# Performance work log

Measured on AMD Instinct MI355X. Metric: run time of the kernel, lower is better.

The kernel has to match this reference:

```python
import jax, jax.numpy as jnp
import numpy as np

BATCH, IN_DIM, GRID, HID, DEPTH = 2048, 128, 128, 256, 7
BN_EPS = 1e-5


def setup_inputs() -> dict:
    key = jax.random.key(0)
    ks = jax.random.split(key, 10)
    x = jax.random.uniform(ks[0], (BATCH, IN_DIM), dtype=jnp.float32)
    grids = jax.random.uniform(ks[1], (DEPTH, IN_DIM, GRID), dtype=jnp.float32)  # torch.rand init
    fs = jax.random.normal(ks[2], (DEPTH, IN_DIM, GRID, HID), dtype=jnp.float32)
    depth_scores = jnp.ones((DEPTH,), dtype=jnp.float32)
    mlp_W = jax.random.normal(ks[3], (3, HID, HID), dtype=jnp.float32) * (1.0 / np.sqrt(HID))
    mlp_b = jnp.zeros((3, HID), dtype=jnp.float32)
    bn_gamma = jnp.ones((3, HID), dtype=jnp.float32)
    bn_beta = jnp.zeros((3, HID), dtype=jnp.float32)
    W_out = jax.random.normal(ks[4], (HID, 1), dtype=jnp.float32) * (1.0 / np.sqrt(HID))
    b_out = jnp.zeros((1,), dtype=jnp.float32)
    return {"x": x, "grids": grids, "fs": fs, "depth_scores": depth_scores,
            "mlp_W": mlp_W, "mlp_b": mlp_b, "bn_gamma": bn_gamma,
            "bn_beta": bn_beta, "W_out": W_out, "b_out": b_out}


def reference(x, grids, fs, depth_scores, mlp_W, mlp_b, bn_gamma, bn_beta, W_out, b_out):
    # per-feature min-max normalization over the batch dim
    xmin = x.min(axis=0, keepdims=True)
    xmax = x.max(axis=0, keepdims=True)
    z = (x - xmin) / (xmax - xmin + 1e-6)  # [B, I]

    outputs = []
    for i in range(DEPTH):
        Bmat = jax.nn.relu(z[:, :, None] - grids[i][None, :, :])  # [B, I, G]
        # (B.unsqueeze(-1) * fs[i]).sum(2).sum(1) == einsum big,igh->bh
        H = jnp.einsum('big,igh->bh', Bmat, fs[i])  # [B, H]
        if i > 0:  # residual accumulation
            H = H + outputs[-1]
        outputs.append(H)
    stacked = jnp.stack(outputs, axis=0)  # [D, B, H]
    w = jax.nn.softmax(depth_scores)  # depth attention
    h = jnp.einsum('d,dbh->bh', w, stacked)

    # MLP head (BatchNorm uses batch stats = training-mode behaviour; Dropout off)
    for j in range(3):
        h = h @ mlp_W[j] + mlp_b[j]
        mean = h.mean(axis=0)
        var = h.var(axis=0)  # biased, matching torch BN normalization
        h = (h - mean) * jax.lax.rsqrt(var + BN_EPS) * bn_gamma[j] + bn_beta[j]
        h = jax.nn.gelu(h, approximate=False)  # torch nn.GELU is exact erf GELU
    return h @ W_out + b_out
```

## Files before the change

kernel.cpp:

```cpp
#include <hip/hip_runtime.h>
#include <hip/hip_bf16.h>

#define BATCH 2048
#define IN_DIM 128
#define GRIDN 128
#define HID 256
#define DEPTH 7

typedef unsigned int u32;
typedef __attribute__((ext_vector_type(8))) short short8;
typedef __attribute__((ext_vector_type(4))) float floatx4;

#define OFF_FST   ((size_t)0)
#define SZ_FST    ((size_t)7*128*256*128*2)
#define OFF_ZT    (OFF_FST + SZ_FST)
#define SZ_ZT     ((size_t)BATCH*IN_DIM*4)
#define OFF_HPRE  (OFF_ZT + SZ_ZT)
#define SZ_HPRE   ((size_t)BATCH*HID*4)
#define OFF_STATS (OFF_HPRE + SZ_HPRE)
#define SZ_STATS  ((size_t)3*2*HID*4)
#define OFF_KEYS  (OFF_STATS + SZ_STATS)
#define SZ_KEYS   ((size_t)256*4)
#define OFF_CW    (OFF_KEYS + SZ_KEYS)
#define SZ_CW     ((size_t)32)
#define OFF_Y1    (OFF_CW + SZ_CW)
#define SZ_Y      ((size_t)BATCH*HID*4)
#define OFF_Y2    (OFF_Y1 + SZ_Y)
#define OFF_Y3    (OFF_Y2 + SZ_Y)

#define FENCE __asm__ volatile("" ::: "memory")
#define WAITV(c) do { __builtin_amdgcn_s_waitcnt(c); FENCE; } while (0)
#define BARR do { FENCE; __builtin_amdgcn_s_barrier(); FENCE; } while (0)
#define VM8 0x0F78
#define VM0 0x0F70

__device__ __forceinline__ void gload_lds16(const void* g, void* l) {
  __builtin_amdgcn_global_load_lds(
      (const __attribute__((address_space(1))) u32*)g,
      (__attribute__((address_space(3))) u32*)l, 16, 0, 0);
}

__device__ __forceinline__ u32 pack2_bf16(float lo, float hi) {
  __hip_bfloat162 b2;
  b2.x = __float2bfloat16(lo);
  b2.y = __float2bfloat16(hi);
  return *reinterpret_cast<u32*>(&b2);
}

__device__ __forceinline__ u32 pk_trunc(float a, float b) {
  return __builtin_amdgcn_perm(__float_as_uint(b), __float_as_uint(a), 0x07060302u);
}

__device__ __forceinline__ float reluc(float v) {
  return __builtin_amdgcn_fmed3f(v, 0.0f, 1.0f);
}

__device__ __forceinline__ float gelu_exact(float x) {
  return 0.5f * x * (1.0f + erff(x * 0.70710678118654752f));
}

__global__ void prep1_kernel(const float* __restrict__ x, u32* __restrict__ keys,
                             const float* __restrict__ depth_scores,
                             float* __restrict__ cw) {
  int t = threadIdx.x;
  int base = blockIdx.x * 256 + t;
  float mn = 1e30f, mx = -1e30f;
#pragma unroll
  for (int j = 0; j < 16; ++j) {
    float v = x[base + j * 16384];
    mn = fminf(mn, v); mx = fmaxf(mx, v);
  }
  __shared__ float smn[256], smx[256];
  smn[t] = mn; smx[t] = mx;
  __syncthreads();
  if (t < 128) {
    mn = fminf(smn[t], smn[t + 128]);
    mx = fmaxf(smx[t], smx[t + 128]);
    int i = base & 127;
    atomicMax(&keys[i], 0x7FFFFFFFu - __float_as_uint(mn));
    atomicMax(&keys[128 + i], __float_as_uint(mx));
  }
  if (blockIdx.x == 0 && t == 0) {
    float m = -1e30f;
    for (int d0 = 0; d0 < DEPTH; ++d0) m = fmaxf(m, depth_scores[d0]);
    float e[DEPTH]; float sum = 0.f;
    for (int d0 = 0; d0 < DEPTH; ++d0) { e[d0] = expf(depth_scores[d0] - m); sum += e[d0]; }
    float cacc = 0.f; float cs[DEPTH];
    for (int d0 = DEPTH - 1; d0 >= 0; --d0) { cacc += e[d0] / sum; cs[d0] = cacc; }
    for (int d0 = 0; d0 < DEPTH; ++d0) cw[d0] = cs[d0];
  }
}

__global__ void prep2_kernel(const float* __restrict__ x, const u32* __restrict__ keys,
                             float* __restrict__ z_t) {
  __shared__ float lds[128 * 65];
  int t = threadIdx.x;
  int b0 = blockIdx.x * 64;
#pragma unroll
  for (int q = 0; q < 32; ++q) {
    int idx = q * 256 + t;
    int b = idx >> 7, i = idx & 127;
    lds[i * 65 + b] = x[(size_t)(b0 + b) * IN_DIM + i];
  }
  __syncthreads();
#pragma unroll
  for (int q = 0; q < 32; ++q) {
    int idx = q * 256 + t;
    int ii = idx >> 6, bb = idx & 63;
    float mnv = __uint_as_float(0x7FFFFFFFu - keys[ii]);
    float mxv = __uint_as_float(keys[128 + ii]);
    float v = (lds[ii * 65 + bb] - mnv) * (1.0f / (mxv - mnv + 1e-6f));
    z_t[(size_t)ii * BATCH + b0 + bb] = v;
  }
}

__global__ void convert_kernel(const float* __restrict__ fs,
                               const float* __restrict__ cw,
                               __hip_bfloat16* __restrict__ fs2) {
  __shared__ __align__(16) float lds[32 * 256];
  int slab = blockIdx.x;
  int t = threadIdx.x;
  int w = t >> 6, l = t & 63;
  float cd = cw[slab >> 7];
  const float* src = fs + (size_t)slab * (GRIDN * HID);
  char* dstb = (char*)fs2 + (size_t)slab * 65536;

  for (int ks = 0; ks < 4; ++ks) {
    const float* s0 = src + (size_t)ks * 32 * HID;
#pragma unroll
    for (int i = 0; i < 8; ++i) {
      int r = w * 8 + i;
      int mask = ((r >> 3) & 3) << 3;
      gload_lds16(s0 + (size_t)r * HID + ((l * 4) ^ mask),
                  (char*)lds + r * 1024);
    }
    WAITV(VM0);
    BARR;
#pragma unroll
    for (int it = 0; it < 4; ++it) {
      int task = t + it * 256;
      int nhalf = task >> 9;
      int q = task & 511;
      int tt = q >> 6, l4 = (q >> 4) & 3, l15 = q & 15;
      int h = nhalf * 128 + tt * 16 + l15;
      int msk = l4 << 3;
      int hx = h ^ msk;
      uint4 pk4;
      {
        float a0 = lds[(l4 * 8 + 0) * 256 + hx];
        float b0 = lds[(l4 * 8 + 1) * 256 + hx];
        float a1 = lds[(l4 * 8 + 2) * 256 + hx];
        float b1 = lds[(l4 * 8 + 3) * 256 + hx];
        float a2 = lds[(l4 * 8 + 4) * 256 + hx];
        float b2 = lds[(l4 * 8 + 5) * 256 + hx];
        float a3 = lds[(l4 * 8 + 6) * 256 + hx];
        float b3 = lds[(l4 * 8 + 7) * 256 + hx];
        pk4.x = pack2_bf16(cd * a0, cd * b0);
        pk4.y = pack2_bf16(cd * a1, cd * b1);
        pk4.z = pack2_bf16(cd * a2, cd * b2);
        pk4.w = pack2_bf16(cd * a3, cd * b3);
      }
      size_t off = (size_t)nhalf * 32768 + (size_t)ks * 8192 +
                   (size_t)tt * 1024 + l4 * 256 + l15 * 16;
      *(uint4*)(dstb + off) = pk4;
    }
    BARR;
  }
}

__launch_bounds__(256, 2)
__global__ void gemm_kernel(const float* __restrict__ z_t,
                            const float* __restrict__ grids,
                            const __hip_bfloat16* __restrict__ fs2,
                            float* __restrict__ h_pre) {
  __shared__ __align__(16) char lds[24576];

  int bx = blockIdx.x;
  int xcd = bx & 7;
  int t6 = bx >> 3;
  int cg2 = t6 >> 4;
  int jb2 = t6 & 15;
  int chunk = xcd + 8 * cg2;
  int slab0 = chunk * 28;
  int mt = jb2 >> 1;
  int nh = jb2 & 1;

  int tid = threadIdx.x;
  int w = tid >> 6, l = tid & 63;
  int l15 = l & 15, l4 = l >> 4;
  int mbase = mt * 256 + w * 64;
  int nbase = nh * 128;

  floatx4 acc[4][8];
#pragma unroll
  for (int a = 0; a < 4; ++a)
#pragma unroll
    for (int b = 0; b < 8; ++b) acc[a][b] = (floatx4)0.f;

  const char* fsb = (const char*)fs2 + (size_t)slab0 * 65536 + (size_t)nh * 32768 +
                    (size_t)w * 2048 + (size_t)l * 16;

  auto stage8 = [&](int u, int bufIdx) {
    const char* srcb = fsb + (size_t)(u >> 2) * 65536 + (size_t)(u & 3) * 8192;
    char* dst = lds + bufIdx * 8192 + w * 2048;
    gload_lds16(srcb, dst);
    gload_lds16(srcb + 1024, dst + 1024);
  };

  float4 zA, zB;
  float4 g0A, g1A, g0B, g1B;
  auto zgload = [&](int s, float4& zv, float4& G0, float4& G1) {
    int slab = slab0 + (s >> 2);
    int iz = slab & 127;
    const float* zp = z_t + (size_t)iz * BATCH + mbase + l15;
    zv.x = zp[0]; zv.y = zp[16]; zv.z = zp[32]; zv.w = zp[48];
    const float* gp = grids + (size_t)slab * GRIDN + (s & 3) * 32 + l4 * 8;
    G0 = *(const float4*)gp;
    G1 = *(const float4*)(gp + 4);
  };

  short8 af[4];
  short8 bf[8];
  auto rdfrag8 = [&](int bufIdx) {
    const char* bp = lds + bufIdx * 8192 + l * 16;
#pragma unroll
    for (int tt = 0; tt < 8; ++tt)
      bf[tt] = *(const short8*)(bp + tt * 1024);
  };
  auto afgen = [&](const float4 zv, const float4 G0, const float4 G1) {
#pragma unroll
    for (int u = 0; u < 4; ++u) {
      float zu = (u == 0) ? zv.x : (u == 1) ? zv.y : (u == 2) ? zv.z : zv.w;
      union { uint4 q; short8 s8; } pk;
      pk.q.x = pk_trunc(reluc(zu - G0.x), reluc(zu - G0.y));
      pk.q.y = pk_trunc(reluc(zu - G0.z), reluc(zu - G0.w));
      pk.q.z = pk_trunc(reluc(zu - G1.x), reluc(zu - G1.y));
      pk.q.w = pk_trunc(reluc(zu - G1.z), reluc(zu - G1.w));
      af[u] = pk.s8;
    }
  };
  auto mfma32 = [&]() {
    __builtin_amdgcn_s_setprio(1);
#pragma unroll
    for (int u = 0; u < 4; ++u)
#pragma unroll
      for (int tt = 0; tt < 8; ++tt)
        acc[u][tt] = __builtin_amdgcn_mfma_f32_16x16x32_bf16(af[u], bf[tt], acc[u][tt], 0, 0, 0);
    __builtin_amdgcn_s_setprio(0);
  };

#define STEP_FULL(S, BUF, STBUF, ZV, G0, G1)                                   \
  do {                                                                         \
    WAITV(VM8); BARR;                                                          \
    stage8((S) + 2, (STBUF)); FENCE;                                           \
    rdfrag8(BUF);                                                              \
    afgen(ZV, G0, G1);                                                         \
    zgload((S) + 2, ZV, G0, G1); FENCE;                                        \
    mfma32();                                                                  \
  } while (0)

  stage8(0, 0); FENCE;
  zgload(0, zA, g0A, g1A); FENCE;
  stage8(1, 1); FENCE;
  zgload(1, zB, g0B, g1B); FENCE;

#pragma unroll 1
  for (int s0 = 0; s0 < 108; s0 += 6) {
    STEP_FULL(s0 + 0, 0, 2, zA, g0A, g1A);
    STEP_FULL(s0 + 1, 1, 0, zB, g0B, g1B);
    STEP_FULL(s0 + 2, 2, 1, zA, g0A, g1A);
    STEP_FULL(s0 + 3, 0, 2, zB, g0B, g1B);
    STEP_FULL(s0 + 4, 1, 0, zA, g0A, g1A);
    STEP_FULL(s0 + 5, 2, 1, zB, g0B, g1B);
  }

  STEP_FULL(108, 0, 2, zA, g0A, g1A);
  STEP_FULL(109, 1, 0, zB, g0B, g1B);
  WAITV(VM8); BARR;
  rdfrag8(2);
  afgen(zA, g0A, g1A);
  mfma32();
  WAITV(VM0); BARR;
  rdfrag8(0);
  afgen(zB, g0B, g1B);
  mfma32();

  int row0 = mbase + l4 * 4;
  int col0 = nbase + l15;
#pragma unroll
  for (int u = 0; u < 4; ++u) {
#pragma unroll
    for (int tt = 0; tt < 8; ++tt) {
      int col = col0 + tt * 16;
#pragma unroll
      for (int r = 0; r < 4; ++r) {
        int row = row0 + u * 16 + r;
        atomicAdd(&h_pre[(size_t)row * HID + col], acc[u][tt][r]);
      }
    }
  }
}

template <int FIRST>
__global__ void mlp_kernel(const float* __restrict__ Xin,
                           const float* __restrict__ statsIn,
                           const float* __restrict__ gamma,
                           const float* __restrict__ beta,
                           const float* __restrict__ W,
                           const float* __restrict__ bias,
                           float* __restrict__ Yout,
                           float* __restrict__ statsOut) {
  __shared__ float Xs[4][HID];
  int br = blockIdx.x, c = threadIdx.x;
  float mean = 0.f, rstd = 1.f, gm = 1.f, bt = 0.f;
  if (!FIRST) {
    float s1 = statsIn[c], s2 = statsIn[HID + c];
    mean = s1 * (1.0f / BATCH);
    float var = s2 * (1.0f / BATCH) - mean * mean;
    rstd = rsqrtf(var + 1e-5f);
    gm = gamma[c]; bt = beta[c];
  }
#pragma unroll
  for (int r = 0; r < 4; ++r) {
    float v = Xin[(size_t)(br * 4 + r) * HID + c];
    if (!FIRST) v = gelu_exact((v - mean) * rstd * gm + bt);
    Xs[r][c] = v;
  }
  __syncthreads();
  float acc[4] = {0, 0, 0, 0};
#pragma unroll 8
  for (int k = 0; k < HID; ++k) {
    float wv = W[(size_t)k * HID + c];
#pragma unroll
    for (int r = 0; r < 4; ++r) acc[r] += Xs[r][k] * wv;
  }
  float bb = bias[c];
  float s1 = 0.f, s2 = 0.f;
#pragma unroll
  for (int r = 0; r < 4; ++r) {
    float y = acc[r] + bb;
    Yout[(size_t)(br * 4 + r) * HID + c] = y;
    s1 += y; s2 += y * y;
  }
  atomicAdd(&statsOut[c], s1);
  atomicAdd(&statsOut[HID + c], s2);
}

__global__ void final_kernel(const float* __restrict__ Y3,
                             const float* __restrict__ statsIn,
                             const float* __restrict__ gamma,
                             const float* __restrict__ beta,
                             const float* __restrict__ W_out,
                             const float* __restrict__ b_out,
                             float* __restrict__ out) {
  int w = threadIdx.x >> 6, l = threadIdx.x & 63;
  int b = blockIdx.x * 4 + w;
  float4 y = *(const float4*)(Y3 + (size_t)b * HID + l * 4);
  float4 wv = *(const float4*)(W_out + l * 4);
  float r4[4] = {y.x, y.y, y.z, y.w};
  float w4[4] = {wv.x, wv.y, wv.z, wv.w};
  float s = 0.f;
  int c0 = l * 4;
#pragma unroll
  for (int q = 0; q < 4; ++q) {
    int c = c0 + q;
    float s1 = statsIn[c], s2 = statsIn[HID + c];
    float mean = s1 * (1.0f / BATCH);
    float var = s2 * (1.0f / BATCH) - mean * mean;
    float rstd = rsqrtf(var + 1e-5f);
    float v = gelu_exact((r4[q] - mean) * rstd * gamma[c] + beta[c]);
    s += v * w4[q];
  }
#pragma unroll
  for (int off = 32; off > 0; off >>= 1) s += __shfl_down(s, off);
  if (l == 0) out[b] = s + b_out[0];
}

extern "C" void kernel_launch(void* const* d_in, const int* in_sizes, int n_in,
                              void* d_out, int out_size, void* d_ws, size_t ws_size,
                              hipStream_t stream) {
  const float* x      = (const float*)d_in[0];
  const float* grids  = (const float*)d_in[1];
  const float* fs     = (const float*)d_in[2];
  const float* dscore = (const float*)d_in[3];
  const float* mlp_W  = (const float*)d_in[4];
  const float* mlp_b  = (const float*)d_in[5];
  const float* bn_g   = (const float*)d_in[6];
  const float* bn_b   = (const float*)d_in[7];
  const float* W_out  = (const float*)d_in[8];
  const float* b_out  = (const float*)d_in[9];
  float* out = (float*)d_out;

  char* ws = (char*)d_ws;
  __hip_bfloat16* fs2 = (__hip_bfloat16*)(ws + OFF_FST);
  float* z_t   = (float*)(ws + OFF_ZT);
  float* h_pre = (float*)(ws + OFF_HPRE);
  float* stats = (float*)(ws + OFF_STATS);
  u32*   keys  = (u32*)(ws + OFF_KEYS);
  float* cw    = (float*)(ws + OFF_CW);
  float* Y1    = (float*)(ws + OFF_Y1);
  float* Y2    = (float*)(ws + OFF_Y2);
  float* Y3    = (float*)(ws + OFF_Y3);

  hipMemsetAsync(h_pre, 0, SZ_HPRE + SZ_STATS + SZ_KEYS, stream);

  prep1_kernel<<<64, 256, 0, stream>>>(x, keys, dscore, cw);
  prep2_kernel<<<32, 256, 0, stream>>>(x, keys, z_t);
  convert_kernel<<<DEPTH * IN_DIM, 256, 0, stream>>>(fs, cw, fs2);
  gemm_kernel<<<512, 256, 0, stream>>>(z_t, grids, fs2, h_pre);

  mlp_kernel<1><<<512, 256, 0, stream>>>(h_pre, nullptr, nullptr, nullptr,
                                         mlp_W, mlp_b, Y1, stats);
  mlp_kernel<0><<<512, 256, 0, stream>>>(Y1, stats, bn_g, bn_b,
                                         mlp_W + 65536, mlp_b + 256, Y2, stats + 512);
  mlp_kernel<0><<<512, 256, 0, stream>>>(Y2, stats + 512, bn_g + 256, bn_b + 256,
                                         mlp_W + 2 * 65536, mlp_b + 2 * 256, Y3, stats + 1024);
  final_kernel<<<512, 256, 0, stream>>>(Y3, stats + 1024, bn_g + 512, bn_b + 512,
                                        W_out, b_out, out);
}
```

Measured before the change: 425.2 us.

## Halve GEMM block tile to 128x128 and double grid for more occupancy

Each GEMM block now covers 128 rows by 128 columns instead of 256 by 128. The four waves are arranged as a 2x2 grid of 64x64 subtiles, and the launch grows from 512 to 1024 blocks. Accumulators drop from 32 to 16 floatx4, and launch bounds ask for 3 blocks per CU, aiming at more parallelism and better latency hiding. The cost is that each staged B tile is reused by half as many rows, so the bf16 fs weight stream is read twice as often overall, with more global and L2 traffic per MFMA.

```diff
diff --git a/kernel.cpp b/kernel.cpp
--- a/kernel.cpp
+++ b/kernel.cpp
@@ -168,7 +168,7 @@
   }
 }
 
-__launch_bounds__(256, 2)
+__launch_bounds__(256, 3)
 __global__ void gemm_kernel(const float* __restrict__ z_t,
                             const float* __restrict__ grids,
                             const __hip_bfloat16* __restrict__ fs2,
@@ -178,8 +178,8 @@
   int bx = blockIdx.x;
   int xcd = bx & 7;
   int t6 = bx >> 3;
-  int cg2 = t6 >> 4;
-  int jb2 = t6 & 15;
+  int cg2 = t6 >> 5;
+  int jb2 = t6 & 31;
   int chunk = xcd + 8 * cg2;
   int slab0 = chunk * 28;
   int mt = jb2 >> 1;
@@ -188,14 +188,16 @@
   int tid = threadIdx.x;
   int w = tid >> 6, l = tid & 63;
   int l15 = l & 15, l4 = l >> 4;
-  int mbase = mt * 256 + w * 64;
-  int nbase = nh * 128;
-
-  floatx4 acc[4][8];
+  int wm = w >> 1;
+  int wn2 = w & 1;
+  int mbase = mt * 128 + wm * 64;
+  int nbase = nh * 128 + wn2 * 64;
+
+  floatx4 acc[4][4];
 #pragma unroll
   for (int a = 0; a < 4; ++a)
 #pragma unroll
-    for (int b = 0; b < 8; ++b) acc[a][b] = (floatx4)0.f;
+    for (int b = 0; b < 4; ++b) acc[a][b] = (floatx4)0.f;
 
   const char* fsb = (const char*)fs2 + (size_t)slab0 * 65536 + (size_t)nh * 32768 +
                     (size_t)w * 2048 + (size_t)l * 16;
@@ -220,12 +222,12 @@
   };
 
   short8 af[4];
-  short8 bf[8];
-  auto rdfrag8 = [&](int bufIdx) {
-    const char* bp = lds + bufIdx * 8192 + l * 16;
-#pragma unroll
-    for (int tt = 0; tt < 8; ++tt)
-      bf[tt] = *(const short8*)(bp + tt * 1024);
+  short8 bf[4];
+  auto rdfrag4 = [&](int bufIdx) {
+    const char* bp = lds + bufIdx * 8192 + wn2 * 4096 + l * 16;
+#pragma unroll
+    for (int j = 0; j < 4; ++j)
+      bf[j] = *(const short8*)(bp + j * 1024);
   };
   auto afgen = [&](const float4 zv, const float4 G0, const float4 G1) {
 #pragma unroll
@@ -239,13 +241,13 @@
       af[u] = pk.s8;
     }
   };
-  auto mfma32 = [&]() {
+  auto mfma16 = [&]() {
     __builtin_amdgcn_s_setprio(1);
 #pragma unroll
     for (int u = 0; u < 4; ++u)
 #pragma unroll
-      for (int tt = 0; tt < 8; ++tt)
-        acc[u][tt] = __builtin_amdgcn_mfma_f32_16x16x32_bf16(af[u], bf[tt], acc[u][tt], 0, 0, 0);
+      for (int j = 0; j < 4; ++j)
+        acc[u][j] = __builtin_amdgcn_mfma_f32_16x16x32_bf16(af[u], bf[j], acc[u][j], 0, 0, 0);
     __builtin_amdgcn_s_setprio(0);
   };
 
@@ -253,10 +255,10 @@
   do {                                                                         \
     WAITV(VM8); BARR;                                                          \
     stage8((S) + 2, (STBUF)); FENCE;                                           \
-    rdfrag8(BUF);                                                              \
+    rdfrag4(BUF);                                                              \
     afgen(ZV, G0, G1);                                                         \
     zgload((S) + 2, ZV, G0, G1); FENCE;                                        \
-    mfma32();                                                                  \
+    mfma16();                                                                  \
   } while (0)
 
   stage8(0, 0); FENCE;
@@ -277,25 +279,25 @@
   STEP_FULL(108, 0, 2, zA, g0A, g1A);
   STEP_FULL(109, 1, 0, zB, g0B, g1B);
   WAITV(VM8); BARR;
-  rdfrag8(2);
+  rdfrag4(2);
   afgen(zA, g0A, g1A);
-  mfma32();
+  mfma16();
   WAITV(VM0); BARR;
-  rdfrag8(0);
+  rdfrag4(0);
   afgen(zB, g0B, g1B);
-  mfma32();
+  mfma16();
 
   int row0 = mbase + l4 * 4;
   int col0 = nbase + l15;
 #pragma unroll
   for (int u = 0; u < 4; ++u) {
 #pragma unroll
-    for (int tt = 0; tt < 8; ++tt) {
-      int col = col0 + tt * 16;
+    for (int j = 0; j < 4; ++j) {
+      int col = col0 + j * 16;
 #pragma unroll
       for (int r = 0; r < 4; ++r) {
         int row = row0 + u * 16 + r;
-        atomicAdd(&h_pre[(size_t)row * HID + col], acc[u][tt][r]);
+        atomicAdd(&h_pre[(size_t)row * HID + col], acc[u][j][r]);
       }
     }
   }
@@ -407,7 +409,7 @@
   prep1_kernel<<<64, 256, 0, stream>>>(x, keys, dscore, cw);
   prep2_kernel<<<32, 256, 0, stream>>>(x, keys, z_t);
   convert_kernel<<<DEPTH * IN_DIM, 256, 0, stream>>>(fs, cw, fs2);
-  gemm_kernel<<<512, 256, 0, stream>>>(z_t, grids, fs2, h_pre);
+  gemm_kernel<<<1024, 256, 0, stream>>>(z_t, grids, fs2, h_pre);
 
   mlp_kernel<1><<<512, 256, 0, stream>>>(h_pre, nullptr, nullptr, nullptr,
                                          mlp_W, mlp_b, Y1, stats);
```

Measured after the change: 433.1 us. Within noise of the previous version (+1.8%).

## Fuse min-max prep into convert kernel and triple-buffer fs conversion loads

Applied to the files above, without the earlier changes.

Merges the min/max reduction kernel into the fs-to-bf16 conversion kernel as extra blocks, and has each conversion block compute its own softmax tail weight instead of reading it from a prior kernel. The conversion loop is restructured from four synchronous 32-row phases into eight 16-row phases with a three-slot LDS ring, so global-to-LDS loads overlap with the bf16 packing work. This removes one launch and a serial dependency, and aims to hide memory latency in a bandwidth-bound conversion of the large fs tensor. The cost is redundant per-block softmax math and more barriers per block.

```diff
diff --git a/kernel.cpp b/kernel.cpp
--- a/kernel.cpp
+++ b/kernel.cpp
@@ -32,6 +32,7 @@
 #define WAITV(c) do { __builtin_amdgcn_s_waitcnt(c); FENCE; } while (0)
 #define BARR do { FENCE; __builtin_amdgcn_s_barrier(); FENCE; } while (0)
 #define VM8 0x0F78
+#define VM4 0x0F74
 #define VM0 0x0F70
 
 __device__ __forceinline__ void gload_lds16(const void* g, void* l) {
@@ -59,36 +60,99 @@
   return 0.5f * x * (1.0f + erff(x * 0.70710678118654752f));
 }
 
-__global__ void prep1_kernel(const float* __restrict__ x, u32* __restrict__ keys,
-                             const float* __restrict__ depth_scores,
-                             float* __restrict__ cw) {
+__global__ void convert_prep1_kernel(const float* __restrict__ fs,
+                                     const float* __restrict__ depth_scores,
+                                     const float* __restrict__ x,
+                                     u32* __restrict__ keys,
+                                     __hip_bfloat16* __restrict__ fs2) {
+  __shared__ __align__(16) float lds3[3 * 16 * 256];
+  int bid = blockIdx.x;
   int t = threadIdx.x;
-  int base = blockIdx.x * 256 + t;
-  float mn = 1e30f, mx = -1e30f;
-#pragma unroll
-  for (int j = 0; j < 16; ++j) {
-    float v = x[base + j * 16384];
-    mn = fminf(mn, v); mx = fmaxf(mx, v);
-  }
-  __shared__ float smn[256], smx[256];
-  smn[t] = mn; smx[t] = mx;
-  __syncthreads();
-  if (t < 128) {
-    mn = fminf(smn[t], smn[t + 128]);
-    mx = fmaxf(smx[t], smx[t + 128]);
-    int i = base & 127;
-    atomicMax(&keys[i], 0x7FFFFFFFu - __float_as_uint(mn));
-    atomicMax(&keys[128 + i], __float_as_uint(mx));
-  }
-  if (blockIdx.x == 0 && t == 0) {
-    float m = -1e30f;
-    for (int d0 = 0; d0 < DEPTH; ++d0) m = fmaxf(m, depth_scores[d0]);
-    float e[DEPTH]; float sum = 0.f;
-    for (int d0 = 0; d0 < DEPTH; ++d0) { e[d0] = expf(depth_scores[d0] - m); sum += e[d0]; }
-    float cacc = 0.f; float cs[DEPTH];
-    for (int d0 = DEPTH - 1; d0 >= 0; --d0) { cacc += e[d0] / sum; cs[d0] = cacc; }
-    for (int d0 = 0; d0 < DEPTH; ++d0) cw[d0] = cs[d0];
-  }
+
+  if (bid >= DEPTH * IN_DIM) {
+    int pb = bid - DEPTH * IN_DIM;
+    int base = pb * 256 + t;
+    float mn = 1e30f, mx = -1e30f;
+#pragma unroll
+    for (int j = 0; j < 16; ++j) {
+      float v = x[base + j * 16384];
+      mn = fminf(mn, v); mx = fmaxf(mx, v);
+    }
+    float* smn = lds3; float* smx = lds3 + 256;
+    smn[t] = mn; smx[t] = mx;
+    __syncthreads();
+    if (t < 128) {
+      mn = fminf(smn[t], smn[t + 128]);
+      mx = fmaxf(smx[t], smx[t + 128]);
+      int i = base & 127;
+      atomicMax(&keys[i], 0x7FFFFFFFu - __float_as_uint(mn));
+      atomicMax(&keys[128 + i], __float_as_uint(mx));
+    }
+    return;
+  }
+
+  int slab = bid;
+  int w = t >> 6, l = t & 63;
+  int d = slab >> 7;
+  float m = -1e30f; float ds[DEPTH];
+#pragma unroll
+  for (int i = 0; i < DEPTH; ++i) { ds[i] = depth_scores[i]; m = fmaxf(m, ds[i]); }
+  float sum = 0.f, tail = 0.f;
+#pragma unroll
+  for (int i = 0; i < DEPTH; ++i) {
+    float e = expf(ds[i] - m);
+    sum += e;
+    if (i >= d) tail += e;
+  }
+  float cd = tail / sum;
+
+  const float* src = fs + (size_t)slab * (GRIDN * HID);
+  char* dstb = (char*)fs2 + (size_t)slab * 65536;
+
+  auto dmaPhase = [&](int p) {
+    const float* s0 = src + (size_t)p * 16 * HID;
+    char* bb = (char*)lds3 + (p % 3) * 16384;
+#pragma unroll
+    for (int i = 0; i < 4; ++i) {
+      int sl = w * 4 + i;
+      int r = p * 16 + sl;
+      int mask = ((r >> 3) & 3) << 3;
+      gload_lds16(s0 + (size_t)sl * HID + ((l * 4) ^ mask), bb + sl * 1024);
+    }
+  };
+  auto packPhase = [&](int p) {
+    int ks = p >> 1, hh = p & 1;
+    const float* bb = lds3 + (p % 3) * 4096;
+#pragma unroll
+    for (int it = 0; it < 2; ++it) {
+      int task = t + it * 256;
+      int nhalf = task >> 8;
+      int q = task & 255;
+      int tt = q >> 5, l4h = (q >> 4) & 1, l15 = q & 15;
+      int l4 = hh * 2 + l4h;
+      int hgl = nhalf * 128 + tt * 16 + l15;
+      int hx = hgl ^ (l4 << 3);
+      const float* rp = bb + (l4h * 8) * 256 + hx;
+      uint4 pk4;
+      pk4.x = pack2_bf16(cd * rp[0 * 256], cd * rp[1 * 256]);
+      pk4.y = pack2_bf16(cd * rp[2 * 256], cd * rp[3 * 256]);
+      pk4.z = pack2_bf16(cd * rp[4 * 256], cd * rp[5 * 256]);
+      pk4.w = pack2_bf16(cd * rp[6 * 256], cd * rp[7 * 256]);
+      size_t off = (size_t)nhalf * 32768 + (size_t)ks * 8192 +
+                   (size_t)tt * 1024 + (size_t)l4 * 256 + (size_t)l15 * 16;
+      *(uint4*)(dstb + off) = pk4;
+    }
+  };
+
+  dmaPhase(0); dmaPhase(1); FENCE;
+#pragma unroll 1
+  for (int p = 0; p < 6; ++p) {
+    WAITV(VM4); BARR;
+    dmaPhase(p + 2); FENCE;
+    packPhase(p);
+  }
+  WAITV(VM4); BARR; packPhase(6);
+  WAITV(VM0); BARR; packPhase(7);
 }
 
 __global__ void prep2_kernel(const float* __restrict__ x, const u32* __restrict__ keys,
@@ -111,60 +175,6 @@
     float mxv = __uint_as_float(keys[128 + ii]);
     float v = (lds[ii * 65 + bb] - mnv) * (1.0f / (mxv - mnv + 1e-6f));
     z_t[(size_t)ii * BATCH + b0 + bb] = v;
-  }
-}
-
-__global__ void convert_kernel(const float* __restrict__ fs,
-                               const float* __restrict__ cw,
-                               __hip_bfloat16* __restrict__ fs2) {
-  __shared__ __align__(16) float lds[32 * 256];
-  int slab = blockIdx.x;
-  int t = threadIdx.x;
-  int w = t >> 6, l = t & 63;
-  float cd = cw[slab >> 7];
-  const float* src = fs + (size_t)slab * (GRIDN * HID);
-  char* dstb = (char*)fs2 + (size_t)slab * 65536;
-
-  for (int ks = 0; ks < 4; ++ks) {
-    const float* s0 = src + (size_t)ks * 32 * HID;
-#pragma unroll
-    for (int i = 0; i < 8; ++i) {
-      int r = w * 8 + i;
-      int mask = ((r >> 3) & 3) << 3;
-      gload_lds16(s0 + (size_t)r * HID + ((l * 4) ^ mask),
-                  (char*)lds + r * 1024);
-    }
-    WAITV(VM0);
-    BARR;
-#pragma unroll
-    for (int it = 0; it < 4; ++it) {
-      int task = t + it * 256;
-      int nhalf = task >> 9;
-      int q = task & 511;
-      int tt = q >> 6, l4 = (q >> 4) & 3, l15 = q & 15;
-      int h = nhalf * 128 + tt * 16 + l15;
-      int msk = l4 << 3;
-      int hx = h ^ msk;
-      uint4 pk4;
-      {
-        float a0 = lds[(l4 * 8 + 0) * 256 + hx];
-        float b0 = lds[(l4 * 8 + 1) * 256 + hx];
-        float a1 = lds[(l4 * 8 + 2) * 256 + hx];
-        float b1 = lds[(l4 * 8 + 3) * 256 + hx];
-        float a2 = lds[(l4 * 8 + 4) * 256 + hx];
-        float b2 = lds[(l4 * 8 + 5) * 256 + hx];
-        float a3 = lds[(l4 * 8 + 6) * 256 + hx];
-        float b3 = lds[(l4 * 8 + 7) * 256 + hx];
-        pk4.x = pack2_bf16(cd * a0, cd * b0);
-        pk4.y = pack2_bf16(cd * a1, cd * b1);
-        pk4.z = pack2_bf16(cd * a2, cd * b2);
-        pk4.w = pack2_bf16(cd * a3, cd * b3);
-      }
-      size_t off = (size_t)nhalf * 32768 + (size_t)ks * 8192 +
-                   (size_t)tt * 1024 + l4 * 256 + l15 * 16;
-      *(uint4*)(dstb + off) = pk4;
-    }
-    BARR;
   }
 }
 
@@ -397,16 +407,15 @@
   float* h_pre = (float*)(ws + OFF_HPRE);
   float* stats = (float*)(ws + OFF_STATS);
   u32*   keys  = (u32*)(ws + OFF_KEYS);
-  float* cw    = (float*)(ws + OFF_CW);
   float* Y1    = (float*)(ws + OFF_Y1);
   float* Y2    = (float*)(ws + OFF_Y2);
   float* Y3    = (float*)(ws + OFF_Y3);
 
   hipMemsetAsync(h_pre, 0, SZ_HPRE + SZ_STATS + SZ_KEYS, stream);
 
-  prep1_kernel<<<64, 256, 0, stream>>>(x, keys, dscore, cw);
+  convert_prep1_kernel<<<DEPTH * IN_DIM + 64, 256, 0, stream>>>(fs, dscore, x,
+                                                                keys, fs2);
   prep2_kernel<<<32, 256, 0, stream>>>(x, keys, z_t);
-  convert_kernel<<<DEPTH * IN_DIM, 256, 0, stream>>>(fs, cw, fs2);
   gemm_kernel<<<512, 256, 0, stream>>>(z_t, grids, fs2, h_pre);
 
   mlp_kernel<1><<<512, 256, 0, stream>>>(h_pre, nullptr, nullptr, nullptr,
```

Result: no change. 425.4 us (+0.0%).
